# Kernel optimization log

Hardware: AMD Instinct MI355X
Metric: run time of the kernel (lower is better)

## Reference

```python
import jax, jax.numpy as jnp
import numpy as np

VOCAB, CTX, EMBED, HEADS = 32000, 2048, 1024, 16


def setup_inputs() -> dict:
    key = jax.random.key(0)
    ks = jax.random.split(key, 10)
    E = EMBED
    s = 0.02
    return {
        "x": jax.random.randint(ks[0], (2, 2048), 0, VOCAB, dtype=jnp.int32),
        "tok_emb": jax.random.normal(ks[1], (VOCAB, E), jnp.float32) * s,
        "pos_emb": jax.random.normal(ks[2], (CTX, E), jnp.float32) * s,
        "qkv_w": jax.random.normal(ks[3], (E, 3 * E), jnp.float32) * s,
        "qkv_b": jnp.zeros((3 * E,), jnp.float32),
        "proj_w": jax.random.normal(ks[4], (E, E), jnp.float32) * s,
        "proj_b": jnp.zeros((E,), jnp.float32),
        "fc_w": jax.random.normal(ks[5], (E, VOCAB), jnp.float32) * s,
        "fc_b": jnp.zeros((VOCAB,), jnp.float32),
    }


def reference(x, tok_emb, pos_emb, qkv_w, qkv_b, proj_w, proj_b, fc_w, fc_b):
    B, T = x.shape
    H = HEADS
    E = tok_emb.shape[1]
    hd = E // H
    h = tok_emb[x] + pos_emb[:T][None, :, :]                      # [B,T,E]
    qkv = h @ qkv_w + qkv_b                                       # [B,T,3E]
    q, k, v = jnp.split(qkv, 3, axis=-1)
    # [B,T,E] -> [B,H,T,hd]
    q = q.reshape(B, T, H, hd).transpose(0, 2, 1, 3)
    k = k.reshape(B, T, H, hd).transpose(0, 2, 1, 3)
    v = v.reshape(B, T, H, hd).transpose(0, 2, 1, 3)
    att = jnp.einsum("bhqd,bhkd->bhqk", q, k) / jnp.sqrt(jnp.float32(hd))
    causal = jnp.tril(jnp.ones((T, T), dtype=bool))
    att = jnp.where(causal[None, None], att, jnp.float32(-jnp.inf))
    att = jax.nn.softmax(att, axis=-1)
    out = jnp.einsum("bhqk,bhkd->bhqd", att, v)                   # [B,H,T,hd]
    out = out.transpose(0, 2, 1, 3).reshape(B, T, E)
    out = out @ proj_w + proj_b
    return out @ fc_w + fc_b                                      # [B,T,VOCAB]
```

## Files before the change

### kernel.cpp

```cpp
#include <hip/hip_runtime.h>

#define BATCH 2
#define T 2048
#define E 1024
#define NH 16
#define HD 64
#define M (BATCH*T)
#define K3 (3*E)
#define VOCAB 32000

typedef __attribute__((ext_vector_type(8))) short s16x8;
typedef __attribute__((ext_vector_type(4))) short s16x4;
typedef __attribute__((ext_vector_type(4))) float f32x4;

__device__ inline unsigned short f2bf(float f) {
  union { float f; unsigned u; } x; x.f = f;
  unsigned r = x.u + 0x7fffu + ((x.u >> 16) & 1u);
  return (unsigned short)(r >> 16);
}

__device__ inline void gload16(const void* g, void* l) {
  __builtin_amdgcn_global_load_lds(
      (const __attribute__((address_space(1))) unsigned int*)g,
      (__attribute__((address_space(3))) unsigned int*)l, 16, 0, 0);
}

__device__ inline void wt_body(const float* __restrict__ W,
    unsigned short* __restrict__ Wt, int N, int n0, int k0, int t,
    float (*tile)[65]) {
  int kl = t >> 2, c = t & 3;
  #pragma unroll
  for (int i = 0; i < 4; i++) {
    float4 v4 = *(const float4*)(W + (size_t)(k0 + kl) * N + n0 + c * 16 + i * 4);
    tile[kl][c * 16 + i * 4 + 0] = v4.x;
    tile[kl][c * 16 + i * 4 + 1] = v4.y;
    tile[kl][c * 16 + i * 4 + 2] = v4.z;
    tile[kl][c * 16 + i * 4 + 3] = v4.w;
  }
  __syncthreads();
  #pragma unroll
  for (int j = 0; j < 2; j++) {
    int idx = t + j * 256;
    int nl = idx >> 3, kq = (idx & 7) * 8;
    s16x8 o;
    #pragma unroll
    for (int i = 0; i < 8; i++) o[i] = (short)f2bf(tile[kq + i][nl]);
    *(s16x8*)(Wt + (size_t)(n0 + nl) * 1024 + k0 + kq) = o;
  }
}

__global__ __launch_bounds__(256) void k_pre(const int* __restrict__ x,
    const float* __restrict__ tok, const float* __restrict__ pos,
    unsigned short* __restrict__ hb,
    const float* __restrict__ qkvw, unsigned short* __restrict__ qkvwt,
    const float* __restrict__ projw, unsigned short* __restrict__ projwt) {
  __shared__ __align__(16) float tile[64][65];
  int gid = blockIdx.x, t = threadIdx.x;
  if (gid < 4096) {
    int row = gid;
    int tt = row & (T - 1);
    int tokid = x[row];
    float4 a = ((const float4*)(tok + (size_t)tokid * E))[t];
    float4 p = ((const float4*)(pos + (size_t)tt * E))[t];
    s16x4 o;
    o[0] = (short)f2bf(a.x + p.x); o[1] = (short)f2bf(a.y + p.y);
    o[2] = (short)f2bf(a.z + p.z); o[3] = (short)f2bf(a.w + p.w);
    *(s16x4*)(hb + (size_t)row * E + t * 4) = o;
    return;
  }
  if (gid < 4864) {
    int idx = gid - 4096;
    wt_body(qkvw, qkvwt, K3, (idx % 48) * 64, (idx / 48) * 64, t, tile);
    return;
  }
  int idx = gid - 4864;
  wt_body(projw, projwt, E, (idx % 16) * 64, (idx / 16) * 64, t, tile);
}

template<int MODE>
__global__ __launch_bounds__(256) void k_bgemm(
    const unsigned short* __restrict__ A, const unsigned short* __restrict__ Bt,
    const float* __restrict__ bias, float* __restrict__ C, int N,
    unsigned short* __restrict__ Cb) {
  __shared__ char lds[16384];
  char* As = lds;
  char* Bs = lds + 8192;
  int tid = threadIdx.x;
  int lane = tid & 63;
  int wv = tid >> 6;
  int wm = wv >> 1, wn = wv & 1;
  int n0 = blockIdx.x * 128, m0 = blockIdx.y * 128;
  int fr = lane & 15, fq = lane >> 4;

  f32x4 acc[4][4];
  #pragma unroll
  for (int i = 0; i < 4; i++)
    #pragma unroll
    for (int j = 0; j < 4; j++) acc[i][j] = (f32x4){0.f, 0.f, 0.f, 0.f};

  int p0 = tid * 16, p1 = tid * 16 + 4096;
  int r0 = p0 >> 6, c0 = p0 & 63;
  int r1 = p1 >> 6, c1 = p1 & 63;
  int cs0 = c0 ^ (((r0 >> 1) & 3) << 4);
  int cs1 = c1 ^ (((r1 >> 1) & 3) << 4);
  const char* ga0 = (const char*)(A + (size_t)(m0 + r0) * 1024) + cs0;
  const char* ga1 = (const char*)(A + (size_t)(m0 + r1) * 1024) + cs1;
  const char* gb0 = (const char*)(Bt + (size_t)(n0 + r0) * 1024) + cs0;
  const char* gb1 = (const char*)(Bt + (size_t)(n0 + r1) * 1024) + cs1;

  int aoff[4], boff[4];
  #pragma unroll
  for (int i = 0; i < 4; i++) {
    int ra = wm * 64 + i * 16 + fr;
    aoff[i] = ra * 64 + ((fq * 16) ^ (((ra >> 1) & 3) << 4));
    int rb = wn * 64 + i * 16 + fr;
    boff[i] = rb * 64 + ((fq * 16) ^ (((rb >> 1) & 3) << 4));
  }

  for (int kb = 0; kb < 2048; kb += 64) {
    gload16(ga0 + kb, As + p0);
    gload16(ga1 + kb, As + p1);
    gload16(gb0 + kb, Bs + p0);
    gload16(gb1 + kb, Bs + p1);
    __syncthreads();
    s16x8 af[4], bfr[4];
    #pragma unroll
    for (int i = 0; i < 4; i++) af[i] = *(const s16x8*)(As + aoff[i]);
    #pragma unroll
    for (int i = 0; i < 4; i++) bfr[i] = *(const s16x8*)(Bs + boff[i]);
    #pragma unroll
    for (int mi = 0; mi < 4; mi++)
      #pragma unroll
      for (int ni = 0; ni < 4; ni++)
        acc[mi][ni] = __builtin_amdgcn_mfma_f32_16x16x32_bf16(
            af[mi], bfr[ni], acc[mi][ni], 0, 0, 0);
    __syncthreads();
  }

  #pragma unroll
  for (int mi = 0; mi < 4; mi++) {
    #pragma unroll
    for (int ni = 0; ni < 4; ni++) {
      #pragma unroll
      for (int j = 0; j < 4; j++) {
        int m = m0 + wm * 64 + mi * 16 + fq * 4 + j;
        int n = n0 + wn * 64 + ni * 16 + fr;
        float val = acc[mi][ni][j] + bias[n];
        if (MODE == 0) C[(size_t)m * N + n] = val;
        else           Cb[(size_t)m * 1024 + n] = f2bf(val);
      }
    }
  }
}

__global__ __launch_bounds__(512, 2) void k_qkv(
    const unsigned short* __restrict__ A, const unsigned short* __restrict__ Bt,
    const float* __restrict__ bias,
    unsigned short* __restrict__ qo, unsigned short* __restrict__ ko,
    unsigned short* __restrict__ vo) {
  __shared__ __align__(16) char lds[131072];
  int tid = threadIdx.x, lane = tid & 63, wv = tid >> 6;
  int WM = wv >> 2, WN = wv & 3;
  int fr = lane & 15, fq = lane >> 4;

  int bid = blockIdx.x;
  int wg = (bid & 7) * 24 + (bid >> 3);
  int m0 = (wg % 16) * 256;
  int n0 = (wg / 16) * 256;

  const char* gA[4]; const char* gB[4]; int lo[4];
  #pragma unroll
  for (int j = 0; j < 4; j++) {
    int i = tid + j * 512;
    int r = i >> 3, c = i & 7;
    int cc = c ^ (r & 7);
    gA[j] = (const char*)A + ((size_t)(m0 + r) * 1024 + cc * 8) * 2;
    gB[j] = (const char*)Bt + ((size_t)(n0 + r) * 1024 + cc * 8) * 2;
    lo[j] = i * 16;
  }

  f32x4 acc[8][4];
  #pragma unroll
  for (int i = 0; i < 8; i++)
    #pragma unroll
    for (int j = 0; j < 4; j++) acc[i][j] = (f32x4){0.f, 0.f, 0.f, 0.f};

  #pragma unroll
  for (int j = 0; j < 4; j++) {
    gload16(gA[j], lds + lo[j]);
    gload16(gB[j], lds + 65536 + lo[j]);
  }
  __syncthreads();

  for (int t = 0; t < 16; t++) {
    int cur = t & 1;
    if (t + 1 < 16) {
      int kb = (t + 1) * 128;
      int nxt = cur ^ 1;
      #pragma unroll
      for (int j = 0; j < 4; j++) {
        gload16(gA[j] + kb, lds + nxt * 32768 + lo[j]);
        gload16(gB[j] + kb, lds + 65536 + nxt * 32768 + lo[j]);
      }
    }
    const char* As = lds + cur * 32768;
    const char* Bs = lds + 65536 + cur * 32768;
    #pragma unroll
    for (int kh = 0; kh < 2; kh++) {
      s16x8 af[8], bf[4];
      #pragma unroll
      for (int mi = 0; mi < 8; mi++) {
        int r = WM * 128 + mi * 16 + fr;
        af[mi] = *(const s16x8*)(As + r * 128 + (((kh * 4 + fq) ^ (r & 7)) << 4));
      }
      #pragma unroll
      for (int ni = 0; ni < 4; ni++) {
        int r = WN * 64 + ni * 16 + fr;
        bf[ni] = *(const s16x8*)(Bs + r * 128 + (((kh * 4 + fq) ^ (r & 7)) << 4));
      }
      __builtin_amdgcn_s_setprio(1);
      #pragma unroll
      for (int mi = 0; mi < 8; mi++)
        #pragma unroll
        for (int ni = 0; ni < 4; ni++)
          acc[mi][ni] = __builtin_amdgcn_mfma_f32_16x16x32_bf16(
              af[mi], bf[ni], acc[mi][ni], 0, 0, 0);
      __builtin_amdgcn_s_setprio(0);
    }
    __syncthreads();
  }

  #pragma unroll
  for (int mi = 0; mi < 8; mi++) {
    #pragma unroll
    for (int ni = 0; ni < 4; ni++) {
      int n = n0 + WN * 64 + ni * 16 + fr;
      int which = n >> 10;
      int e = n & (E - 1);
      int hh = e >> 6, d = e & 63;
      int mb = m0 + WM * 128 + mi * 16 + fq * 4;
      int b = mb >> 11, tt0 = mb & (T - 1);
      float bv = bias[n];
      if (which == 2) {
        s16x4 pk;
        #pragma unroll
        for (int j = 0; j < 4; j++) pk[j] = (short)f2bf(acc[mi][ni][j] + bv);
        *(s16x4*)(vo + ((size_t)(b * NH + hh) * 64 + d) * T + tt0) = pk;
      } else {
        unsigned short* dst = (which == 0) ? qo : ko;
        #pragma unroll
        for (int j = 0; j < 4; j++)
          dst[((size_t)(b * NH + hh) * T + tt0 + j) * 64 + d] =
              f2bf(acc[mi][ni][j] + bv);
      }
    }
  }
}

__global__ __launch_bounds__(512, 2) void k_fc(
    const unsigned short* __restrict__ A, const unsigned short* __restrict__ Bt,
    const float* __restrict__ bias, float* __restrict__ C) {
  __shared__ __align__(16) char lds[131072];
  int tid = threadIdx.x, lane = tid & 63, wv = tid >> 6;
  int WM = wv >> 2, WN = wv & 3;
  int fr = lane & 15, fq = lane >> 4;

  int bid = blockIdx.x;
  int wg = (bid & 7) * 250 + (bid >> 3);
  int m0 = (wg & 15) * 256;
  int n0 = (wg >> 4) * 256;

  const char* gA[4]; const char* gB[4]; int lo[4];
  #pragma unroll
  for (int j = 0; j < 4; j++) {
    int i = tid + j * 512;
    int r = i >> 3, c = i & 7;
    int cc = c ^ (r & 7);
    gA[j] = (const char*)A + ((size_t)(m0 + r) * 1024 + cc * 8) * 2;
    gB[j] = (const char*)Bt + ((size_t)(n0 + r) * 1024 + cc * 8) * 2;
    lo[j] = i * 16;
  }

  f32x4 acc[8][4];
  #pragma unroll
  for (int i = 0; i < 8; i++)
    #pragma unroll
    for (int j = 0; j < 4; j++) acc[i][j] = (f32x4){0.f, 0.f, 0.f, 0.f};

  #pragma unroll
  for (int j = 0; j < 4; j++) {
    gload16(gA[j], lds + lo[j]);
    gload16(gB[j], lds + 65536 + lo[j]);
  }
  __syncthreads();

  for (int t = 0; t < 16; t++) {
    int cur = t & 1;
    if (t + 1 < 16) {
      int kb = (t + 1) * 128;
      int nxt = cur ^ 1;
      #pragma unroll
      for (int j = 0; j < 4; j++) {
        gload16(gA[j] + kb, lds + nxt * 32768 + lo[j]);
        gload16(gB[j] + kb, lds + 65536 + nxt * 32768 + lo[j]);
      }
    }
    const char* As = lds + cur * 32768;
    const char* Bs = lds + 65536 + cur * 32768;
    #pragma unroll
    for (int kh = 0; kh < 2; kh++) {
      s16x8 af[8], bf[4];
      #pragma unroll
      for (int mi = 0; mi < 8; mi++) {
        int r = WM * 128 + mi * 16 + fr;
        af[mi] = *(const s16x8*)(As + r * 128 + (((kh * 4 + fq) ^ (r & 7)) << 4));
      }
      #pragma unroll
      for (int ni = 0; ni < 4; ni++) {
        int r = WN * 64 + ni * 16 + fr;
        bf[ni] = *(const s16x8*)(Bs + r * 128 + (((kh * 4 + fq) ^ (r & 7)) << 4));
      }
      __builtin_amdgcn_s_setprio(1);
      #pragma unroll
      for (int mi = 0; mi < 8; mi++)
        #pragma unroll
        for (int ni = 0; ni < 4; ni++)
          acc[mi][ni] = __builtin_amdgcn_mfma_f32_16x16x32_bf16(
              af[mi], bf[ni], acc[mi][ni], 0, 0, 0);
      __builtin_amdgcn_s_setprio(0);
    }
    __syncthreads();
  }

  #pragma unroll
  for (int mi = 0; mi < 8; mi++) {
    #pragma unroll
    for (int ni = 0; ni < 4; ni++) {
      int n = n0 + WN * 64 + ni * 16 + fr;
      float bv = bias[n];
      #pragma unroll
      for (int j = 0; j < 4; j++) {
        int m = m0 + WM * 128 + mi * 16 + fq * 4 + j;
        C[(size_t)m * VOCAB + n] = acc[mi][ni][j] + bv;
      }
    }
  }
}

#define BM 128
#define BN 128
#define BKF 32
#define LDT (BM + 4)
__global__ __launch_bounds__(256) void k_gemm32(
    const float* __restrict__ A, const float* __restrict__ Bw,
    const float* __restrict__ bias, float* __restrict__ C, int N) {
  __shared__ float As[BKF * LDT];
  __shared__ float Bs[BKF * LDT];
  int tid = threadIdx.x;
  int tx = tid & 15, ty = tid >> 4;
  int n0 = blockIdx.x * BN;
  int m0 = blockIdx.y * BM;
  float acc[8][8];
  #pragma unroll
  for (int i = 0; i < 8; i++)
    #pragma unroll
    for (int j = 0; j < 8; j++) acc[i][j] = 0.f;
  for (int k0 = 0; k0 < E; k0 += BKF) {
    #pragma unroll
    for (int i = 0; i < 4; i++) {
      int f = i * 256 + tid;
      int ml = f >> 3, c4 = f & 7;
      float4 va = *(const float4*)(A + (size_t)(m0 + ml) * E + k0 + c4 * 4);
      As[(c4 * 4 + 0) * LDT + ml] = va.x;
      As[(c4 * 4 + 1) * LDT + ml] = va.y;
      As[(c4 * 4 + 2) * LDT + ml] = va.z;
      As[(c4 * 4 + 3) * LDT + ml] = va.w;
    }
    #pragma unroll
    for (int i = 0; i < 4; i++) {
      int f = i * 256 + tid;
      int kk = f >> 5, c4 = f & 31;
      float4 vb = *(const float4*)(Bw + (size_t)(k0 + kk) * N + n0 + c4 * 4);
      *(float4*)(Bs + kk * LDT + c4 * 4) = vb;
    }
    __syncthreads();
    #pragma unroll
    for (int kk = 0; kk < BKF; kk++) {
      const float4* ar = (const float4*)(As + kk * LDT);
      const float4* br = (const float4*)(Bs + kk * LDT);
      float4 a0 = ar[ty * 2], a1 = ar[ty * 2 + 1];
      float4 b0 = br[tx * 2], b1 = br[tx * 2 + 1];
      float av[8] = {a0.x, a0.y, a0.z, a0.w, a1.x, a1.y, a1.z, a1.w};
      float bvv[8] = {b0.x, b0.y, b0.z, b0.w, b1.x, b1.y, b1.z, b1.w};
      #pragma unroll
      for (int i = 0; i < 8; i++)
        #pragma unroll
        for (int j = 0; j < 8; j++)
          acc[i][j] = fmaf(av[i], bvv[j], acc[i][j]);
    }
    __syncthreads();
  }
  int mbase = m0 + ty * 8;
  int nbase = n0 + tx * 8;
  #pragma unroll
  for (int i = 0; i < 8; i++) {
    float* crow = C + (size_t)(mbase + i) * N + nbase;
    #pragma unroll
    for (int j = 0; j < 8; j++) crow[j] = acc[i][j] + bias[nbase + j];
  }
}

__global__ __launch_bounds__(256) void k_attn_wt(
    const unsigned short* __restrict__ qb, const unsigned short* __restrict__ kb,
    const unsigned short* __restrict__ vtb, unsigned short* __restrict__ o,
    const float* __restrict__ fcw, unsigned short* __restrict__ fcwt) {
  __shared__ __align__(16) char lds[49152];
  int gid = blockIdx.x;
  int tid = threadIdx.x;

  if (gid >= 512) {
    int idx = gid - 512;
    wt_body(fcw, fcwt, VOCAB, (idx % 500) * 64, (idx / 500) * 64, tid,
            (float(*)[65])lds);
    return;
  }

  int qt = 15 - (gid >> 5);
  int bh = gid & 31;
  int b = bh >> 4, hh = bh & 15;
  int lane = tid & 63, wv = tid >> 6;
  int fr = lane & 15, fq = lane >> 4;
  int q0 = qt * 128;
  int qw0 = q0 + wv * 32;
  const char* Kg = (const char*)(kb + (size_t)bh * T * 64);
  const char* Vg = (const char*)(vtb + (size_t)bh * 64 * T);
  char* Pl = lds + 32768 + wv * 4096;

  s16x8 qf[2][2];
  #pragma unroll
  for (int g = 0; g < 2; g++) {
    const unsigned short* Qg = qb + ((size_t)bh * T + qw0 + g * 16) * 64;
    qf[g][0] = *(const s16x8*)(Qg + (size_t)fr * 64 + fq * 8);
    qf[g][1] = *(const s16x8*)(Qg + (size_t)fr * 64 + 32 + fq * 8);
  }

  f32x4 po[2][4];
  float mrow[2][4], lrow[2][4];
  #pragma unroll
  for (int g = 0; g < 2; g++)
    #pragma unroll
    for (int j = 0; j < 4; j++) {
      po[g][j] = (f32x4){0.f, 0.f, 0.f, 0.f};
      mrow[g][j] = -1e30f; lrow[g][j] = 0.f;
    }

  int ntiles = qt * 2 + 2;
  int i0 = tid, i1 = tid + 256;
  int sr0 = i0 >> 3, sc0 = ((i0 & 7) ^ (sr0 & 7)) << 4;
  int sr1 = i1 >> 3, sc1 = ((i1 & 7) ^ (sr1 & 7)) << 4;

  {
    gload16(Kg + (size_t)sr0 * 128 + sc0, lds + i0 * 16);
    gload16(Kg + (size_t)sr1 * 128 + sc1, lds + i1 * 16);
    gload16(Vg + (size_t)sr0 * (T * 2) + sc0, lds + 16384 + i0 * 16);
    gload16(Vg + (size_t)sr1 * (T * 2) + sc1, lds + 16384 + i1 * 16);
  }
  __syncthreads();
  int cur = 0;

  for (int kt = 0; kt < ntiles; kt++) {
    int kv0 = kt * 64;
    if (kt + 1 < ntiles) {
      size_t kvn = (size_t)(kv0 + 64);
      char* kd = lds + (cur ^ 1) * 8192;
      char* vd = lds + 16384 + (cur ^ 1) * 8192;
      gload16(Kg + (kvn + sr0) * 128 + sc0, kd + i0 * 16);
      gload16(Kg + (kvn + sr1) * 128 + sc1, kd + i1 * 16);
      gload16(Vg + (size_t)sr0 * (T * 2) + kvn * 2 + sc0, vd + i0 * 16);
      gload16(Vg + (size_t)sr1 * (T * 2) + kvn * 2 + sc1, vd + i1 * 16);
    }
    const char* Kt = lds + cur * 8192;
    const char* Vt = lds + 16384 + cur * 8192;

    f32x4 s[2][4];
    #pragma unroll
    for (int ni = 0; ni < 4; ni++) {
      int r = ni * 16 + fr;
      s16x8 kf0 = *(const s16x8*)(Kt + r * 128 + ((fq ^ (r & 7)) << 4));
      s16x8 kf1 = *(const s16x8*)(Kt + r * 128 + (((4 + fq) ^ (r & 7)) << 4));
      #pragma unroll
      for (int g = 0; g < 2; g++) {
        s[g][ni] = (f32x4){0.f, 0.f, 0.f, 0.f};
        s[g][ni] = __builtin_amdgcn_mfma_f32_16x16x32_bf16(qf[g][0], kf0, s[g][ni], 0, 0, 0);
        s[g][ni] = __builtin_amdgcn_mfma_f32_16x16x32_bf16(qf[g][1], kf1, s[g][ni], 0, 0, 0);
      }
    }

    #pragma unroll
    for (int g = 0; g < 2; g++) {
      int qw = qw0 + g * 16;
      bool needm = (kv0 + 63 > qw);
      #pragma unroll
      for (int jj = 0; jj < 4; jj++) {
        int row = qw + fq * 4 + jj;
        float tm = -1e30f;
        #pragma unroll
        for (int ni = 0; ni < 4; ni++) {
          float val = s[g][ni][jj] * 0.125f;
          if (needm) { int col = kv0 + ni * 16 + fr; if (col > row) val = -1e30f; }
          s[g][ni][jj] = val;
          tm = fmaxf(tm, val);
        }
        #pragma unroll
        for (int mk = 1; mk < 16; mk <<= 1) tm = fmaxf(tm, __shfl_xor(tm, mk));
        if (__any(tm > mrow[g][jj] + 8.f)) {
          float nm = fmaxf(mrow[g][jj], tm);
          float corr = __expf(mrow[g][jj] - nm);
          mrow[g][jj] = nm;
          #pragma unroll
          for (int ni = 0; ni < 4; ni++) po[g][ni][jj] *= corr;
          lrow[g][jj] *= corr;
        }
        float mref = mrow[g][jj];
        float rs = 0.f;
        #pragma unroll
        for (int ni = 0; ni < 4; ni++) {
          float pv = __expf(s[g][ni][jj] - mref);
          s[g][ni][jj] = pv;
          rs += pv;
        }
        #pragma unroll
        for (int mk = 1; mk < 16; mk <<= 1) rs += __shfl_xor(rs, mk);
        lrow[g][jj] += rs;
      }
    }

    asm volatile("s_waitcnt lgkmcnt(0)" ::: "memory");
    #pragma unroll
    for (int g = 0; g < 2; g++) {
      char* Pg = Pl + g * 2048;
      #pragma unroll
      for (int ni = 0; ni < 4; ni++) {
        int col = ni * 16 + fr;
        #pragma unroll
        for (int jj = 0; jj < 4; jj++) {
          int qq = fq * 4 + jj;
          *(unsigned short*)(Pg + qq * 128 + (((col >> 3) ^ (qq & 7)) << 4) +
                             (col & 7) * 2) = f2bf(s[g][ni][jj]);
        }
      }
    }
    asm volatile("s_waitcnt lgkmcnt(0)" ::: "memory");

    s16x8 pa[2][2];
    #pragma unroll
    for (int g = 0; g < 2; g++) {
      const char* Pg = Pl + g * 2048;
      pa[g][0] = *(const s16x8*)(Pg + fr * 128 + ((fq ^ (fr & 7)) << 4));
      pa[g][1] = *(const s16x8*)(Pg + fr * 128 + (((4 + fq) ^ (fr & 7)) << 4));
    }
    #pragma unroll
    for (int ni = 0; ni < 4; ni++) {
      int r = ni * 16 + fr;
      s16x8 vf0 = *(const s16x8*)(Vt + r * 128 + ((fq ^ (r & 7)) << 4));
      s16x8 vf1 = *(const s16x8*)(Vt + r * 128 + (((4 + fq) ^ (r & 7)) << 4));
      #pragma unroll
      for (int g = 0; g < 2; g++) {
        po[g][ni] = __builtin_amdgcn_mfma_f32_16x16x32_bf16(pa[g][0], vf0, po[g][ni], 0, 0, 0);
        po[g][ni] = __builtin_amdgcn_mfma_f32_16x16x32_bf16(pa[g][1], vf1, po[g][ni], 0, 0, 0);
      }
    }
    __syncthreads();
    cur ^= 1;
  }

  #pragma unroll
  for (int g = 0; g < 2; g++)
    #pragma unroll
    for (int jj = 0; jj < 4; jj++) {
      float inv = 1.f / lrow[g][jj];
      int row = qw0 + g * 16 + fq * 4 + jj;
      unsigned short* orow = o + ((size_t)(b * T + row)) * E + hh * 64;
      #pragma unroll
      for (int ni = 0; ni < 4; ni++)
        orow[ni * 16 + fr] = f2bf(po[g][ni][jj] * inv);
    }
}

extern "C" void kernel_launch(void* const* d_in, const int* in_sizes, int n_in,
                              void* d_out, int out_size, void* d_ws, size_t ws_size,
                              hipStream_t stream) {
  const int*   x      = (const int*)d_in[0];
  const float* tok    = (const float*)d_in[1];
  const float* pos    = (const float*)d_in[2];
  const float* qkv_w  = (const float*)d_in[3];
  const float* qkv_b  = (const float*)d_in[4];
  const float* proj_w = (const float*)d_in[5];
  const float* proj_b = (const float*)d_in[6];
  const float* fc_w   = (const float*)d_in[7];
  const float* fc_b   = (const float*)d_in[8];
  float* out = (float*)d_out;
  float* ws  = (float*)d_ws;

  unsigned short* hb      = (unsigned short*)out;
  unsigned short* qkv_wt  = (unsigned short*)(out + 2097152);
  unsigned short* qbuf    = (unsigned short*)(out + 3670016);
  unsigned short* kbuf    = (unsigned short*)(out + 5767168);
  unsigned short* vtbuf   = (unsigned short*)(out + 7864320);
  unsigned short* aob     = (unsigned short*)(out + 9961472);
  unsigned short* proj_wt = (unsigned short*)(out + 12058624);

  const size_t WS_FAST = (size_t)(2097152 + 16384000) * 4;

  k_pre<<<5120, 256, 0, stream>>>(x, tok, pos, hb, qkv_w, qkv_wt, proj_w, proj_wt);
  k_qkv<<<192, 512, 0, stream>>>(hb, qkv_wt, qkv_b, qbuf, kbuf, vtbuf);

  if (ws_size >= WS_FAST) {
    unsigned short* h2b   = (unsigned short*)ws;
    unsigned short* fc_wt = (unsigned short*)(ws + 2097152);
    k_attn_wt<<<8512, 256, 0, stream>>>(qbuf, kbuf, vtbuf, aob, fc_w, fc_wt);
    k_bgemm<2><<<dim3(E / 128, M / 128), 256, 0, stream>>>(
        aob, proj_wt, proj_b, nullptr, E, h2b);
    k_fc<<<dim3((M / 256) * (VOCAB / 256)), 512, 0, stream>>>(
        h2b, fc_wt, fc_b, out);
  } else {
    float* h2 = ws;
    k_attn_wt<<<512, 256, 0, stream>>>(qbuf, kbuf, vtbuf, aob, nullptr, nullptr);
    k_bgemm<0><<<dim3(E / 128, M / 128), 256, 0, stream>>>(
        aob, proj_wt, proj_b, h2, E, nullptr);
    k_gemm32<<<dim3(VOCAB / BN, M / BM), 256, 0, stream>>>(
        h2, fc_w, fc_b, out, VOCAB);
  }
}
```

Baseline: 501.7 us.

## Switch FC GEMM to 32x32x16 MFMA and defer attention max reduction

The vocab projection GEMM now uses 32x32x16 bf16 MFMA tiles instead of 16x16x32, with the fragment loads and output index mapping reorganised to match. Larger MFMA tiles need fewer LDS fragment reads per FLOP and fewer instructions to issue. In the attention softmax, the cross-lane max shuffle reduction now runs only when a rescale is actually triggered; the trigger test uses each lane's local max, which is still correct because __any sees whether any lane exceeds the threshold.

```diff
diff --git a/kernel.cpp b/kernel.cpp
--- a/kernel.cpp
+++ b/kernel.cpp
@@ -12,6 +12,7 @@
 typedef __attribute__((ext_vector_type(8))) short s16x8;
 typedef __attribute__((ext_vector_type(4))) short s16x4;
 typedef __attribute__((ext_vector_type(4))) float f32x4;
+typedef __attribute__((ext_vector_type(16))) float f32x16;
 
 __device__ inline unsigned short f2bf(float f) {
   union { float f; unsigned u; } x; x.f = f;
@@ -263,7 +264,7 @@
   __shared__ __align__(16) char lds[131072];
   int tid = threadIdx.x, lane = tid & 63, wv = tid >> 6;
   int WM = wv >> 2, WN = wv & 3;
-  int fr = lane & 15, fq = lane >> 4;
+  int l31 = lane & 31, lh = lane >> 5;
 
   int bid = blockIdx.x;
   int wg = (bid & 7) * 250 + (bid >> 3);
@@ -281,11 +282,13 @@
     lo[j] = i * 16;
   }
 
-  f32x4 acc[8][4];
-  #pragma unroll
-  for (int i = 0; i < 8; i++)
-    #pragma unroll
-    for (int j = 0; j < 4; j++) acc[i][j] = (f32x4){0.f, 0.f, 0.f, 0.f};
+  f32x16 acc[4][2];
+  #pragma unroll
+  for (int i = 0; i < 4; i++)
+    #pragma unroll
+    for (int j = 0; j < 2; j++)
+      #pragma unroll
+      for (int e = 0; e < 16; e++) acc[i][j][e] = 0.f;
 
   #pragma unroll
   for (int j = 0; j < 4; j++) {
@@ -309,39 +312,49 @@
     const char* Bs = lds + 65536 + cur * 32768;
     #pragma unroll
     for (int kh = 0; kh < 2; kh++) {
-      s16x8 af[8], bf[4];
-      #pragma unroll
-      for (int mi = 0; mi < 8; mi++) {
-        int r = WM * 128 + mi * 16 + fr;
-        af[mi] = *(const s16x8*)(As + r * 128 + (((kh * 4 + fq) ^ (r & 7)) << 4));
-      }
-      #pragma unroll
-      for (int ni = 0; ni < 4; ni++) {
-        int r = WN * 64 + ni * 16 + fr;
-        bf[ni] = *(const s16x8*)(Bs + r * 128 + (((kh * 4 + fq) ^ (r & 7)) << 4));
+      s16x8 af[4][2], bf[2][2];
+      #pragma unroll
+      for (int mb = 0; mb < 4; mb++) {
+        int r = WM * 128 + mb * 32 + l31;
+        #pragma unroll
+        for (int ks = 0; ks < 2; ks++) {
+          int ch = kh * 4 + ks * 2 + lh;
+          af[mb][ks] = *(const s16x8*)(As + r * 128 + ((ch ^ (r & 7)) << 4));
+        }
+      }
+      #pragma unroll
+      for (int nb = 0; nb < 2; nb++) {
+        int r = WN * 64 + nb * 32 + l31;
+        #pragma unroll
+        for (int ks = 0; ks < 2; ks++) {
+          int ch = kh * 4 + ks * 2 + lh;
+          bf[nb][ks] = *(const s16x8*)(Bs + r * 128 + ((ch ^ (r & 7)) << 4));
+        }
       }
       __builtin_amdgcn_s_setprio(1);
       #pragma unroll
-      for (int mi = 0; mi < 8; mi++)
-        #pragma unroll
-        for (int ni = 0; ni < 4; ni++)
-          acc[mi][ni] = __builtin_amdgcn_mfma_f32_16x16x32_bf16(
-              af[mi], bf[ni], acc[mi][ni], 0, 0, 0);
+      for (int mb = 0; mb < 4; mb++)
+        #pragma unroll
+        for (int nb = 0; nb < 2; nb++)
+          #pragma unroll
+          for (int ks = 0; ks < 2; ks++)
+            acc[mb][nb] = __builtin_amdgcn_mfma_f32_32x32x16_bf16(
+                af[mb][ks], bf[nb][ks], acc[mb][nb], 0, 0, 0);
       __builtin_amdgcn_s_setprio(0);
     }
     __syncthreads();
   }
 
   #pragma unroll
-  for (int mi = 0; mi < 8; mi++) {
-    #pragma unroll
-    for (int ni = 0; ni < 4; ni++) {
-      int n = n0 + WN * 64 + ni * 16 + fr;
+  for (int mb = 0; mb < 4; mb++) {
+    #pragma unroll
+    for (int nb = 0; nb < 2; nb++) {
+      int n = n0 + WN * 64 + nb * 32 + l31;
       float bv = bias[n];
       #pragma unroll
-      for (int j = 0; j < 4; j++) {
-        int m = m0 + WM * 128 + mi * 16 + fq * 4 + j;
-        C[(size_t)m * VOCAB + n] = acc[mi][ni][j] + bv;
+      for (int reg = 0; reg < 16; reg++) {
+        int m = m0 + WM * 128 + mb * 32 + (reg & 3) + 8 * (reg >> 2) + 4 * lh;
+        C[(size_t)m * VOCAB + n] = acc[mb][nb][reg] + bv;
       }
     }
   }
@@ -511,10 +524,11 @@
           s[g][ni][jj] = val;
           tm = fmaxf(tm, val);
         }
-        #pragma unroll
-        for (int mk = 1; mk < 16; mk <<= 1) tm = fmaxf(tm, __shfl_xor(tm, mk));
         if (__any(tm > mrow[g][jj] + 8.f)) {
-          float nm = fmaxf(mrow[g][jj], tm);
+          float twm = tm;
+          #pragma unroll
+          for (int mk = 1; mk < 16; mk <<= 1) twm = fmaxf(twm, __shfl_xor(twm, mk));
+          float nm = fmaxf(mrow[g][jj], twm);
           float corr = __expf(mrow[g][jj] - nm);
           mrow[g][jj] = nm;
           #pragma unroll
```

Result: no change. 493.0 us (median of 3 runs) (-1.7%).
